# Kernel optimization log

Hardware: AMD Instinct MI355X
Metric: run time of the kernel (lower is better)

## Reference

```python
import jax, jax.numpy as jnp
import numpy as np

B = 16
DRUG_LEN, PROT_LEN = 64, 1200
DIM, CONV = 64, 40


def conv1d(x, w, b):
    # x: [B, C_in, L], w: [C_out, C_in, K] (torch layout), VALID padding
    y = jax.lax.conv_general_dilated(
        x, w, window_strides=(1,), padding='VALID',
        dimension_numbers=('NCH', 'OIH', 'NCH'))
    return y + b[None, :, None]


def setup_inputs() -> dict:
    key = jax.random.key(0)
    ks = jax.random.split(key, 32)
    s = 0.05
    inp = {
        'drug_tokens': jax.random.randint(ks[0], (B, DRUG_LEN), 0, 65, dtype=jnp.int32),
        'protein_tokens': jax.random.randint(ks[1], (B, PROT_LEN), 0, 26, dtype=jnp.int32),
        'drug_emb': (jax.random.normal(ks[2], (65, DIM)) * s).at[0].set(0.0),
        'prot_emb': (jax.random.normal(ks[3], (26, DIM)) * s).at[0].set(0.0),
        'dW1': jax.random.normal(ks[4], (CONV, DIM, 4)) * s,
        'db1': jax.random.normal(ks[5], (CONV,)) * s,
        'dW2': jax.random.normal(ks[6], (CONV * 2, CONV, 6)) * s,
        'db2': jax.random.normal(ks[7], (CONV * 2,)) * s,
        'dW3': jax.random.normal(ks[8], (CONV * 4, CONV * 2, 8)) * s,
        'db3': jax.random.normal(ks[9], (CONV * 4,)) * s,
        'pW1': jax.random.normal(ks[10], (CONV, DIM, 4)) * s,
        'pb1': jax.random.normal(ks[11], (CONV,)) * s,
        'pW2': jax.random.normal(ks[12], (CONV * 2, CONV, 8)) * s,
        'pb2': jax.random.normal(ks[13], (CONV * 2,)) * s,
        'pW3': jax.random.normal(ks[14], (CONV * 4, CONV * 2, 12)) * s,
        'pb3': jax.random.normal(ks[15], (CONV * 4,)) * s,
        'dattW': jax.random.normal(ks[16], (160, 160)) * s,
        'dattb': jax.random.normal(ks[17], (160,)) * s,
        'pattW': jax.random.normal(ks[18], (160, 160)) * s,
        'pattb': jax.random.normal(ks[19], (160,)) * s,
        'attW': jax.random.normal(ks[20], (160, 160)) * s,
        'attb': jax.random.normal(ks[21], (160,)) * s,
        'fc1W': jax.random.normal(ks[22], (1024, 320)) * s,
        'fc1b': jax.random.normal(ks[23], (1024,)) * s,
        'fc2W': jax.random.normal(ks[24], (1024, 1024)) * s,
        'fc2b': jax.random.normal(ks[25], (1024,)) * s,
        'fc3W': jax.random.normal(ks[26], (512, 1024)) * s,
        'fc3b': jax.random.normal(ks[27], (512,)) * s,
        'outW': jax.random.normal(ks[28], (2, 512)) * s,
        'outb': jax.random.normal(ks[29], (2,)) * s,
    }
    return inp


def reference(drug_tokens, protein_tokens, drug_emb, prot_emb,
              dW1, db1, dW2, db2, dW3, db3,
              pW1, pb1, pW2, pb2, pW3, pb3,
              dattW, dattb, pattW, pattb, attW, attb,
              fc1W, fc1b, fc2W, fc2b, fc3W, fc3b, outW, outb):
    relu = jax.nn.relu
    # Embedding lookup, then to [B, C, L]
    de = drug_emb[drug_tokens].transpose(0, 2, 1)    # [B,64,64]
    pe = prot_emb[protein_tokens].transpose(0, 2, 1)  # [B,64,1200]
    # CNN stacks
    dc = relu(conv1d(relu(conv1d(relu(conv1d(de, dW1, db1)), dW2, db2)), dW3, db3))  # [B,160,49]
    pc = relu(conv1d(relu(conv1d(relu(conv1d(pe, pW1, pb1)), pW2, pb2)), pW3, pb3))  # [B,160,1179]
    # Per-token attention projections (Linear over channel dim)
    d_att = jnp.einsum('bcd,oc->bdo', dc, dattW) + dattb   # [B,49,160]
    p_att = jnp.einsum('bcp,oc->bpo', pc, pattW) + pattb   # [B,1179,160]
    # Broadcast outer-sum + ReLU + Linear  -> [B,49,1179,160]
    A = relu(d_att[:, :, None, :] + p_att[:, None, :, :])
    A = jnp.einsum('bdpk,ok->bdpo', A, attW) + attb
    comp_atte = jax.nn.sigmoid(jnp.mean(A, axis=2)).transpose(0, 2, 1)  # [B,160,49]
    prot_atte = jax.nn.sigmoid(jnp.mean(A, axis=1)).transpose(0, 2, 1)  # [B,160,1179]
    dc = dc * 0.5 + dc * comp_atte
    pc = pc * 0.5 + pc * prot_atte
    # Global max pool over length
    dvec = jnp.max(dc, axis=2)  # [B,160]
    pvec = jnp.max(pc, axis=2)  # [B,160]
    pair = jnp.concatenate([dvec, pvec], axis=1)  # [B,320]
    # MLP head (dropout = identity at inference)
    h = jax.nn.leaky_relu(pair @ fc1W.T + fc1b, 0.01)
    h = jax.nn.leaky_relu(h @ fc2W.T + fc2b, 0.01)
    h = jax.nn.leaky_relu(h @ fc3W.T + fc3b, 0.01)
    return h @ outW.T + outb  # [B,2]
```

## Files before the change

kernel.cpp:

```cpp
#include <hip/hip_runtime.h>
#include <hip/hip_bf16.h>

typedef __hip_bfloat16 bf16;
typedef __attribute__((ext_vector_type(8))) short short8;
typedef __attribute__((ext_vector_type(4))) float floatx4;

#define NB 16


__device__ __forceinline__ float b2f(bf16 x) { return __bfloat162float(x); }
__device__ __forceinline__ float u16bf(unsigned short u) {
    return __uint_as_float(((unsigned)u) << 16);
}
__device__ __forceinline__ unsigned short f2bu(float v) {
    union { bf16 h; unsigned short u; } cv;
    cv.h = __float2bfloat16(v);
    return cv.u;
}

__global__ void sniff_kernel(const unsigned short* __restrict__ w, int* __restrict__ flag) {
    __shared__ int cnt;
    if (threadIdx.x == 0) cnt = 0;
    __syncthreads();
    int hits = 0;
    for (int s = 0; s < 4; s++) {
        unsigned short u = w[(threadIdx.x * 4 + s) * 2];
        float v = fabsf(u16bf(u));
        if (v > 1e-6f && v < 2.0f) hits++;
    }
    atomicAdd(&cnt, hits);
    __syncthreads();
    if (threadIdx.x == 0) *flag = (cnt > 512) ? 1 : 0;
}

#define NSEG 14
struct CvtJob {
    const void* src[NSEG];
    float* dst[NSEG];
};
#define NPK 11
struct PackJob {
    const void* src[NPK];
    bf16* dst[NPK];
    short Cout[NPK], CIN[NPK], K[NPK], coP[NPK], CIP[NPK];
};
struct PrepOff { int off[NSEG + NPK + 1]; };

__global__ void prep(CvtJob cj, PackJob pj, PrepOff po, const int* __restrict__ flagp) {
    int g = blockIdx.x * 256 + threadIdx.x;
    if (g >= po.off[NSEG + NPK]) return;
    int s = 0;
#pragma unroll
    for (int t = 1; t < NSEG + NPK; t++)
        if (g >= po.off[t]) s = t;
    int i = g - po.off[s];
    if (s < NSEG) {
        const void* sp = cj.src[s];
        if (sp == nullptr) { cj.dst[s][i] = 0.f; return; }
        cj.dst[s][i] = (*flagp) ? b2f(((const bf16*)sp)[i]) : ((const float*)sp)[i];
    } else {
        int p = s - NSEG;
        int Cout = pj.Cout[p], CIN = pj.CIN[p], K = pj.K[p];
        int coP = pj.coP[p], CIP = pj.CIP[p];
        (void)K;
        int ci = i % CIP;
        int t = i / CIP;
        int co = t % coP;
        int k = t / coP;
        float v = 0.f;
        if (co < Cout && ci < CIN) {
            int si = (co * CIN + ci) * pj.K[p] + k;
            v = (*flagp) ? b2f(((const bf16*)pj.src[p])[si]) : ((const float*)pj.src[p])[si];
        }
        pj.dst[p][i] = __float2bfloat16(v);
    }
}

template <int K, int CIN, int CHUNKS, int NW>
__device__ __forceinline__ void conv_body(unsigned short* xT,
                                          const unsigned short* xb,
                                          const unsigned short* wbase,
                                          const float* __restrict__ bias,
                                          bf16* __restrict__ y,
                                          int b, int Lin, int Lstride, int Lout,
                                          int Cout, int coP, int l0) {
    const int CIP = CHUNKS * 32;
    const int PCI = CIP + 8;
    const int TLX = 64 + K - 1;
    const int LV = (TLX + 7) >> 3;
    for (int i = threadIdx.x; i < CIP * LV; i += NW * 64) {
        int ci = i / LV, lv = (i - ci * LV) << 3;
        if (ci < CIN && lv + 8 <= TLX && l0 + lv + 8 <= Lin) {
            short8 v = *(const short8*)(xb + ci * Lstride + l0 + lv);
#pragma unroll
            for (int j = 0; j < 8; j++) xT[(lv + j) * PCI + ci] = (unsigned short)v[j];
        } else {
            for (int j = 0; j < 8; j++) {
                int l = lv + j;
                if (l >= TLX) break;
                int gl = l0 + l;
                xT[l * PCI + ci] = (ci < CIN && gl < Lin) ? xb[ci * Lstride + gl]
                                                          : (unsigned short)0;
            }
        }
    }
    __syncthreads();
    int lane = threadIdx.x & 63;
    int ct = threadIdx.x >> 6;
    int n = lane & 15, quad = lane >> 4;
    floatx4 acc[4];
#pragma unroll
    for (int i = 0; i < 4; i++) acc[i] = (floatx4){0.f, 0.f, 0.f, 0.f};
#pragma unroll
    for (int k = 0; k < K; k++) {
#pragma unroll
        for (int ch = 0; ch < CHUNKS; ch++) {
            short8 a = *(const short8*)(wbase +
                        ((size_t)(k * coP + ct * 16 + n)) * CIP + ch * 32 + quad * 8);
#pragma unroll
            for (int nt = 0; nt < 4; nt++) {
                short8 bb = *(const short8*)(xT + (nt * 16 + n + k) * PCI + ch * 32 + quad * 8);
                acc[nt] = __builtin_amdgcn_mfma_f32_16x16x32_bf16(a, bb, acc[nt], 0, 0, 0);
            }
        }
    }
    int m0 = quad * 4;
#pragma unroll
    for (int nt = 0; nt < 4; nt++) {
        int l = l0 + nt * 16 + n;
        if (l >= Lout) continue;
#pragma unroll
        for (int r = 0; r < 4; r++) {
            int co = ct * 16 + m0 + r;
            if (co < Cout)
                y[((size_t)b * Cout + co) * Lout + l] =
                    __float2bfloat16(fmaxf(acc[nt][r] + bias[co], 0.f));
        }
    }
}

template <int KD, int KP, int CIN, int CHUNKS, int NW>
__global__ __launch_bounds__(NW * 64) void conv_dual(const bf16* __restrict__ xd,
                                                 const bf16* __restrict__ Wpd,
                                                 const float* __restrict__ bd,
                                                 bf16* __restrict__ yd,
                                                 int LinD, int LsD, int LoutD,
                                                 const bf16* __restrict__ xp,
                                                 const bf16* __restrict__ Wpp,
                                                 const float* __restrict__ bp,
                                                 bf16* __restrict__ yp,
                                                 int LinP, int LsP, int LoutP,
                                                 int Cout, int coP) {
    const int CIP = CHUNKS * 32;
    const int PCI = CIP + 8;
    const int TLXMAX = 64 + KP - 1;
    __shared__ __align__(16) unsigned short xT[TLXMAX * PCI];
    if (blockIdx.x < 16) {
        int b = blockIdx.x;
        conv_body<KD, CIN, CHUNKS, NW>(xT, (const unsigned short*)xd + (size_t)b * CIN * LsD,
                                   (const unsigned short*)Wpd, bd, yd, b, LinD, LsD, LoutD,
                                   Cout, coP, 0);
    } else {
        int bx = blockIdx.x - 16;
        int b = bx / 19, l0 = (bx % 19) << 6;
        conv_body<KP, CIN, CHUNKS, NW>(xT, (const unsigned short*)xp + (size_t)b * CIN * LsP,
                                   (const unsigned short*)Wpp, bp, yp, b, LinP, LsP, LoutP,
                                   Cout, coP, l0);
    }
}

template <int K, int CIN, int CHUNKS, int NW>
__device__ __forceinline__ void conv_proj_phase(unsigned short* xT, unsigned short* xP,
                                                const unsigned short* xb,
                                                const unsigned short* wbase,
                                                const float* __restrict__ bias,
                                                unsigned short* __restrict__ y,
                                                int b, int Lin, int Lout,
                                                int Cout, int coP, int l0) {
    const int CIP = CHUNKS * 32;
    const int PCI = CIP + 8;
    const int TLX = 64 + K - 1;
    const int LV = (TLX + 7) >> 3;
    for (int i = threadIdx.x; i < CIP * LV; i += NW * 64) {
        int ci = i / LV, lv = (i - ci * LV) << 3;
        if (ci < CIN && lv + 8 <= TLX && l0 + lv + 8 <= Lin) {
            short8 v = *(const short8*)(xb + ci * Lin + l0 + lv);
#pragma unroll
            for (int j = 0; j < 8; j++) xT[(lv + j) * PCI + ci] = (unsigned short)v[j];
        } else {
            for (int j = 0; j < 8; j++) {
                int l = lv + j;
                if (l >= TLX) break;
                int gl = l0 + l;
                xT[l * PCI + ci] = (ci < CIN && gl < Lin) ? xb[ci * Lin + gl]
                                                          : (unsigned short)0;
            }
        }
    }
    __syncthreads();
    int lane = threadIdx.x & 63;
    int ct = threadIdx.x >> 6;
    int n = lane & 15, quad = lane >> 4;
    floatx4 acc[4];
#pragma unroll
    for (int i = 0; i < 4; i++) acc[i] = (floatx4){0.f, 0.f, 0.f, 0.f};
#pragma unroll
    for (int k = 0; k < K; k++) {
#pragma unroll
        for (int ch = 0; ch < CHUNKS; ch++) {
            short8 a = *(const short8*)(wbase +
                        ((size_t)(k * coP + ct * 16 + n)) * CIP + ch * 32 + quad * 8);
#pragma unroll
            for (int nt = 0; nt < 4; nt++) {
                short8 bb = *(const short8*)(xT + (nt * 16 + n + k) * PCI + ch * 32 + quad * 8);
                acc[nt] = __builtin_amdgcn_mfma_f32_16x16x32_bf16(a, bb, acc[nt], 0, 0, 0);
            }
        }
    }
    int m0 = quad * 4;
#pragma unroll
    for (int nt = 0; nt < 4; nt++) {
        int ll = nt * 16 + n;
        int l = l0 + ll;
#pragma unroll
        for (int r = 0; r < 4; r++) {
            int co = ct * 16 + m0 + r;
            float val = (l < Lout) ? fmaxf(acc[nt][r] + bias[co], 0.f) : 0.f;
            unsigned short u = f2bu(val);
            xP[ll * 168 + co] = u;
            if (l < Lout) y[((size_t)b * Cout + co) * Lout + l] = u;
        }
    }
}

template <int KD, int KP, int CIN, int CHUNKS, int NW>
__global__ __launch_bounds__(NW * 64) void conv3_proj(
        const bf16* __restrict__ xd, const bf16* __restrict__ Wpd,
        const float* __restrict__ bd, bf16* __restrict__ yd, int LinD, int LoutD,
        const bf16* __restrict__ xp, const bf16* __restrict__ Wpp,
        const float* __restrict__ bp, bf16* __restrict__ yp, int LinP, int LoutP,
        int Cout, int coP,
        const bf16* __restrict__ dWB, const bf16* __restrict__ pWB,
        const float* __restrict__ dbF, const float* __restrict__ pbF,
        float* __restrict__ datt, bf16* __restrict__ pattB) {
    const int CIP = CHUNKS * 32;
    const int PCI = CIP + 8;
    const int TLXMAX = 64 + KP - 1;
    __shared__ __align__(16) unsigned short xT[TLXMAX * PCI];
    __shared__ __align__(16) unsigned short xP[64 * 168];
    bool isD = blockIdx.x < 16;
    int b, l0, L;
    if (isD) {
        b = blockIdx.x; l0 = 0; L = LoutD;
        conv_proj_phase<KD, CIN, CHUNKS, NW>(xT, xP,
            (const unsigned short*)xd + (size_t)b * CIN * LinD,
            (const unsigned short*)Wpd, bd, (unsigned short*)yd, b, LinD, LoutD, Cout, coP, 0);
    } else {
        int bx = blockIdx.x - 16;
        b = bx / 19; l0 = (bx % 19) << 6; L = LoutP;
        conv_proj_phase<KP, CIN, CHUNKS, NW>(xT, xP,
            (const unsigned short*)xp + (size_t)b * CIN * LinP,
            (const unsigned short*)Wpp, bp, (unsigned short*)yp, b, LinP, LoutP, Cout, coP, l0);
    }
    __syncthreads();
    int lane = threadIdx.x & 63;
    int t = threadIdx.x >> 6;
    int n = lane & 15, quad = lane >> 4;
    const unsigned short* W = (const unsigned short*)(isD ? dWB : pWB);
    const float* pbias = isD ? dbF : pbF;
    floatx4 acc[4];
#pragma unroll
    for (int i = 0; i < 4; i++) acc[i] = (floatx4){0.f, 0.f, 0.f, 0.f};
#pragma unroll
    for (int ch = 0; ch < 5; ch++) {
        short8 a = *(const short8*)(W + ((size_t)(t * 16 + n)) * 160 + ch * 32 + quad * 8);
#pragma unroll
        for (int nt = 0; nt < 4; nt++) {
            short8 bb = *(const short8*)(xP + (nt * 16 + n) * 168 + ch * 32 + quad * 8);
            acc[nt] = __builtin_amdgcn_mfma_f32_16x16x32_bf16(a, bb, acc[nt], 0, 0, 0);
        }
    }
    int m0 = quad * 4;
    int o0 = t * 16 + m0;
#pragma unroll
    for (int nt = 0; nt < 4; nt++) {
        int l = l0 + nt * 16 + n;
        if (l >= L) continue;
        if (isD) {
            float4 v;
            v.x = acc[nt][0] + pbias[o0 + 0];
            v.y = acc[nt][1] + pbias[o0 + 1];
            v.z = acc[nt][2] + pbias[o0 + 2];
            v.w = acc[nt][3] + pbias[o0 + 3];
            *(float4*)(datt + ((size_t)b * 49 + l) * 160 + o0) = v;
        } else {
            ushort4 u;
            u.x = f2bu(acc[nt][0] + pbias[o0 + 0]);
            u.y = f2bu(acc[nt][1] + pbias[o0 + 1]);
            u.z = f2bu(acc[nt][2] + pbias[o0 + 2]);
            u.w = f2bu(acc[nt][3] + pbias[o0 + 3]);
            *(ushort4*)((unsigned short*)pattB + ((size_t)b * 1179 + l) * 160 + o0) = u;
        }
    }
}

__global__ __launch_bounds__(256) void conv1_mfma(const int* __restrict__ dtok,
                                                  const int* __restrict__ ptok,
                                                  const bf16* __restrict__ embDB,
                                                  const bf16* __restrict__ embPB,
                                                  const bf16* __restrict__ dW1p,
                                                  const bf16* __restrict__ pW1p,
                                                  const float* __restrict__ db1f,
                                                  const float* __restrict__ pb1f,
                                                  bf16* __restrict__ d1,
                                                  bf16* __restrict__ p1) {
    const int K = 4, CIP = 64, PCI = 72, TLX = 67, coP = 48, Cout = 40;
    __shared__ __align__(16) unsigned short xT[TLX * PCI];
    __shared__ int stok[TLX];
    bool isD = blockIdx.x < 16;
    int b, l0, Lin, Lout, Ostride;
    const int* tok; const unsigned short* embB; const unsigned short* Wp;
    const float* bias; bf16* y;
    if (isD) {
        b = blockIdx.x; l0 = 0; Lin = 64; Lout = 61; Ostride = 62;
        tok = dtok; embB = (const unsigned short*)embDB;
        Wp = (const unsigned short*)dW1p; bias = db1f; y = d1;
    } else {
        int bx = blockIdx.x - 16;
        b = bx / 19; l0 = (bx % 19) << 6; Lin = 1200; Lout = 1197; Ostride = 1198;
        tok = ptok; embB = (const unsigned short*)embPB;
        Wp = (const unsigned short*)pW1p; bias = pb1f; y = p1;
    }
    if (threadIdx.x < TLX) {
        int l = l0 + threadIdx.x;
        stok[threadIdx.x] = (l < Lin) ? tok[b * Lin + l] : -1;
    }
    __syncthreads();
    for (int i = threadIdx.x; i < TLX * 8; i += 256) {
        int l = i >> 3, c8 = (i & 7) << 3;
        int t = stok[l];
        short8 v = (short8){0, 0, 0, 0, 0, 0, 0, 0};
        if (t >= 0) v = *(const short8*)(embB + t * 64 + c8);
        *(short8*)(xT + l * PCI + c8) = v;
    }
    __syncthreads();
    int lane = threadIdx.x & 63;
    int w = threadIdx.x >> 6;
    int n = lane & 15, quad = lane >> 4;
    if (w >= 3) return;
    floatx4 acc[4];
#pragma unroll
    for (int i = 0; i < 4; i++) acc[i] = (floatx4){0.f, 0.f, 0.f, 0.f};
#pragma unroll
    for (int k = 0; k < K; k++) {
#pragma unroll
        for (int ch = 0; ch < 2; ch++) {
            short8 a = *(const short8*)(Wp +
                        ((size_t)(k * coP + w * 16 + n)) * CIP + ch * 32 + quad * 8);
#pragma unroll
            for (int nt = 0; nt < 4; nt++) {
                short8 bb = *(const short8*)(xT + (nt * 16 + n + k) * PCI + ch * 32 + quad * 8);
                acc[nt] = __builtin_amdgcn_mfma_f32_16x16x32_bf16(a, bb, acc[nt], 0, 0, 0);
            }
        }
    }
    int m0 = quad * 4;
#pragma unroll
    for (int nt = 0; nt < 4; nt++) {
        int l = l0 + nt * 16 + n;
        if (l >= Lout) continue;
#pragma unroll
        for (int r = 0; r < 4; r++) {
            int co = w * 16 + m0 + r;
            if (co < Cout)
                y[((size_t)b * Cout + co) * Ostride + l] =
                    __float2bfloat16(fmaxf(acc[nt][r] + bias[co], 0.f));
        }
    }
}

__global__ __launch_bounds__(640) void mean_fused(const float* __restrict__ datt,
                                                  const bf16* __restrict__ patt,
                                                  bf16* __restrict__ MpW,
                                                  float* __restrict__ Mdpart) {
    __shared__ __align__(16) unsigned short sp[37 * 160];
    int tid = threadIdx.x;
    int b = blockIdx.x >> 5;
    int pc = blockIdx.x & 31;
    int p0 = pc * 37;
    int pmax = 1179 - p0;
    if (pmax > 37) pmax = 37;
    {
        const short8* src = (const short8*)((const unsigned short*)patt +
                                            ((size_t)b * 1179 + p0) * 160);
        short8* dst = (short8*)sp;
        int n8 = (pmax * 160) >> 3;
        for (int v = tid; v < n8; v += 640) dst[v] = src[v];
    }
    int h = tid & 3;
    int k = tid >> 2;
    int d0 = h * 13;
    int nd = (h == 3) ? 10 : 13;
    const float* drow = datt + (size_t)b * 49 * 160 + k;
    float dv[13], md[13];
#pragma unroll
    for (int i = 0; i < 13; i++) {
        dv[i] = (i < nd) ? drow[(d0 + i) * 160] : -1e30f;
        md[i] = 0.f;
    }
    __syncthreads();
    unsigned short* mp = (unsigned short*)MpW + ((size_t)b * 1184 + p0) * 160 + k;
#pragma unroll 2
    for (int pi = 0; pi < pmax; pi++) {
        float pv = u16bf(sp[pi * 160 + k]);
        float s0 = 0.f, s1 = 0.f, s2 = 0.f, s3 = 0.f;
#pragma unroll
        for (int g = 0; g < 3; g++) {
            float r0 = fmaxf(dv[g * 4 + 0] + pv, 0.f);
            float r1 = fmaxf(dv[g * 4 + 1] + pv, 0.f);
            float r2 = fmaxf(dv[g * 4 + 2] + pv, 0.f);
            float r3 = fmaxf(dv[g * 4 + 3] + pv, 0.f);
            md[g * 4 + 0] += r0; s0 += r0;
            md[g * 4 + 1] += r1; s1 += r1;
            md[g * 4 + 2] += r2; s2 += r2;
            md[g * 4 + 3] += r3; s3 += r3;
        }
        {
            float r = fmaxf(dv[12] + pv, 0.f);
            md[12] += r; s0 += r;
        }
        float s = (s0 + s1) + (s2 + s3);
        s += __shfl_xor(s, 1, 64);
        s += __shfl_xor(s, 2, 64);
        if (h == 0) mp[(size_t)pi * 160] = f2bu(s * (1.f / 49.f));
    }
    float* op = Mdpart + (((size_t)b * 32 + pc) * 49) * 160 + k;
#pragma unroll
    for (int i = 0; i < 13; i++)
        if (i < nd) op[(d0 + i) * 160] = md[i];
}

__global__ __launch_bounds__(640) void att_sig_mfma(const float* __restrict__ Mdpart,
                                                    const bf16* __restrict__ MpW,
                                                    const bf16* __restrict__ wattB,
                                                    const float* __restrict__ attbF,
                                                    const bf16* __restrict__ dcB,
                                                    const bf16* __restrict__ pcB,
                                                    float* __restrict__ pair) {
    const int PCI = 168;
    __shared__ __align__(16) unsigned short sM[64 * PCI];
    bool isD = blockIdx.x < 16;
    int b, p0, L, off;
    const unsigned short* conv;
    if (isD) {
        b = blockIdx.x; p0 = 0; L = 49; off = 0; conv = (const unsigned short*)dcB;
        const float* mdp = Mdpart + (size_t)b * 32 * 49 * 160;
        for (int i = threadIdx.x; i < 160 * 64; i += 640) {
            int r = i / 160, k = i - r * 160;
            float v = 0.f;
            if (r < 49) {
                const float* src = mdp + r * 160 + k;
                float s0 = 0.f, s1 = 0.f, s2 = 0.f, s3 = 0.f;
#pragma unroll
                for (int pc = 0; pc < 32; pc += 4) {
                    s0 += src[(size_t)(pc + 0) * 7840];
                    s1 += src[(size_t)(pc + 1) * 7840];
                    s2 += src[(size_t)(pc + 2) * 7840];
                    s3 += src[(size_t)(pc + 3) * 7840];
                }
                v = ((s0 + s1) + (s2 + s3)) * (1.f / 1179.f);
            }
            sM[r * PCI + k] = f2bu(v);
        }
    } else {
        int bx = blockIdx.x - 16;
        b = bx / 19; p0 = (bx % 19) << 6; L = 1179; off = 160;
        conv = (const unsigned short*)pcB;
        const unsigned short* mb = (const unsigned short*)MpW + (size_t)b * 1184 * 160;
        for (int i = threadIdx.x; i < 160 * 64; i += 640) {
            int r = i / 160, k = i - r * 160;
            int p = p0 + r;
            sM[r * PCI + k] = (p < 1179) ? mb[(size_t)p * 160 + k] : (unsigned short)0;
        }
    }
    __syncthreads();
    int lane = threadIdx.x & 63;
    int t = threadIdx.x >> 6;
    int n = lane & 15, quad = lane >> 4;
    floatx4 acc[4];
#pragma unroll
    for (int i = 0; i < 4; i++) acc[i] = (floatx4){0.f, 0.f, 0.f, 0.f};
    const unsigned short* W = (const unsigned short*)wattB;
#pragma unroll
    for (int ch = 0; ch < 5; ch++) {
        short8 a = *(const short8*)(W + ((size_t)(t * 16 + n)) * 160 + ch * 32 + quad * 8);
#pragma unroll
        for (int nt = 0; nt < 4; nt++) {
            short8 bb = *(const short8*)(sM + (nt * 16 + n) * PCI + ch * 32 + quad * 8);
            acc[nt] = __builtin_amdgcn_mfma_f32_16x16x32_bf16(a, bb, acc[nt], 0, 0, 0);
        }
    }
    int m0 = quad * 4;
    float vmax[4] = {0.f, 0.f, 0.f, 0.f};
#pragma unroll
    for (int nt = 0; nt < 4; nt++) {
        int p = p0 + nt * 16 + n;
#pragma unroll
        for (int r = 0; r < 4; r++) {
            int o = t * 16 + m0 + r;
            float sig = 1.f / (1.f + __expf(-(acc[nt][r] + attbF[o])));
            float v = 0.f;
            if (p < L) v = u16bf(conv[((size_t)b * 160 + o) * L + p]) * (0.5f + sig);
            vmax[r] = fmaxf(vmax[r], v);
        }
    }
#pragma unroll
    for (int m = 1; m < 16; m <<= 1) {
#pragma unroll
        for (int r = 0; r < 4; r++)
            vmax[r] = fmaxf(vmax[r], __shfl_xor(vmax[r], m, 64));
    }
    if (n == 0) {
#pragma unroll
        for (int r = 0; r < 4; r++)
            atomicMax((unsigned int*)(pair + b * 320 + off + t * 16 + m0 + r),
                      __float_as_uint(vmax[r]));
    }
}

__global__ __launch_bounds__(256) void fc_block(const float* __restrict__ in,
                                                const void* __restrict__ W,
                                                const float* __restrict__ bias,
                                                float* __restrict__ out,
                                                int IN, int OUT,
                                                const int* __restrict__ flagp) {
    int j = blockIdx.x;
    int w = threadIdx.x >> 6, li = threadIdx.x & 63;
    int nv = IN >> 2;
    const float4* i0 = (const float4*)(in + (size_t)(w * 4 + 0) * IN);
    const float4* i1 = (const float4*)(in + (size_t)(w * 4 + 1) * IN);
    const float4* i2 = (const float4*)(in + (size_t)(w * 4 + 2) * IN);
    const float4* i3 = (const float4*)(in + (size_t)(w * 4 + 3) * IN);
    float p0 = 0.f, p1 = 0.f, p2 = 0.f, p3 = 0.f;
    if (*flagp) {
        const ushort4* w4 = (const ushort4*)((const unsigned short*)W + (size_t)j * IN);
        for (int v = li; v < nv; v += 64) {
            ushort4 u = w4[v];
            float wa = u16bf(u.x), wb = u16bf(u.y), wc = u16bf(u.z), wd = u16bf(u.w);
            float4 x;
            x = i0[v]; p0 += x.x * wa + x.y * wb + x.z * wc + x.w * wd;
            x = i1[v]; p1 += x.x * wa + x.y * wb + x.z * wc + x.w * wd;
            x = i2[v]; p2 += x.x * wa + x.y * wb + x.z * wc + x.w * wd;
            x = i3[v]; p3 += x.x * wa + x.y * wb + x.z * wc + x.w * wd;
        }
    } else {
        const float4* w4 = (const float4*)((const float*)W + (size_t)j * IN);
        for (int v = li; v < nv; v += 64) {
            float4 u = w4[v];
            float4 x;
            x = i0[v]; p0 += x.x * u.x + x.y * u.y + x.z * u.z + x.w * u.w;
            x = i1[v]; p1 += x.x * u.x + x.y * u.y + x.z * u.z + x.w * u.w;
            x = i2[v]; p2 += x.x * u.x + x.y * u.y + x.z * u.z + x.w * u.w;
            x = i3[v]; p3 += x.x * u.x + x.y * u.y + x.z * u.z + x.w * u.w;
        }
    }
#pragma unroll
    for (int m = 1; m < 64; m <<= 1) {
        p0 += __shfl_xor(p0, m, 64);
        p1 += __shfl_xor(p1, m, 64);
        p2 += __shfl_xor(p2, m, 64);
        p3 += __shfl_xor(p3, m, 64);
    }
    if (li == 0) {
        float bj = bias[j];
        float o0 = p0 + bj, o1 = p1 + bj, o2 = p2 + bj, o3 = p3 + bj;
        o0 = o0 > 0.f ? o0 : 0.01f * o0;
        o1 = o1 > 0.f ? o1 : 0.01f * o1;
        o2 = o2 > 0.f ? o2 : 0.01f * o2;
        o3 = o3 > 0.f ? o3 : 0.01f * o3;
        out[(size_t)(w * 4 + 0) * OUT + j] = o0;
        out[(size_t)(w * 4 + 1) * OUT + j] = o1;
        out[(size_t)(w * 4 + 2) * OUT + j] = o2;
        out[(size_t)(w * 4 + 3) * OUT + j] = o3;
    }
}

__global__ __launch_bounds__(256) void out_block(const float* __restrict__ h,
                                                 const void* __restrict__ W,
                                                 const float* __restrict__ biasF,
                                                 void* __restrict__ out,
                                                 const int* __restrict__ flagp) {
    int j = blockIdx.x;
    int w = threadIdx.x >> 6, li = threadIdx.x & 63;
    const int IN = 512, nv = 128;
    const float4* i0 = (const float4*)(h + (size_t)(w * 4 + 0) * IN);
    const float4* i1 = (const float4*)(h + (size_t)(w * 4 + 1) * IN);
    const float4* i2 = (const float4*)(h + (size_t)(w * 4 + 2) * IN);
    const float4* i3 = (const float4*)(h + (size_t)(w * 4 + 3) * IN);
    float p0 = 0.f, p1 = 0.f, p2 = 0.f, p3 = 0.f;
    int flag = *flagp;
    if (flag) {
        const ushort4* w4 = (const ushort4*)((const unsigned short*)W + (size_t)j * IN);
        for (int v = li; v < nv; v += 64) {
            ushort4 u = w4[v];
            float wa = u16bf(u.x), wb = u16bf(u.y), wc = u16bf(u.z), wd = u16bf(u.w);
            float4 x;
            x = i0[v]; p0 += x.x * wa + x.y * wb + x.z * wc + x.w * wd;
            x = i1[v]; p1 += x.x * wa + x.y * wb + x.z * wc + x.w * wd;
            x = i2[v]; p2 += x.x * wa + x.y * wb + x.z * wc + x.w * wd;
            x = i3[v]; p3 += x.x * wa + x.y * wb + x.z * wc + x.w * wd;
        }
    } else {
        const float4* w4 = (const float4*)((const float*)W + (size_t)j * IN);
        for (int v = li; v < nv; v += 64) {
            float4 u = w4[v];
            float4 x;
            x = i0[v]; p0 += x.x * u.x + x.y * u.y + x.z * u.z + x.w * u.w;
            x = i1[v]; p1 += x.x * u.x + x.y * u.y + x.z * u.z + x.w * u.w;
            x = i2[v]; p2 += x.x * u.x + x.y * u.y + x.z * u.z + x.w * u.w;
            x = i3[v]; p3 += x.x * u.x + x.y * u.y + x.z * u.z + x.w * u.w;
        }
    }
#pragma unroll
    for (int m = 1; m < 64; m <<= 1) {
        p0 += __shfl_xor(p0, m, 64);
        p1 += __shfl_xor(p1, m, 64);
        p2 += __shfl_xor(p2, m, 64);
        p3 += __shfl_xor(p3, m, 64);
    }
    if (li == 0) {
        float bj = biasF[j];
        float o0 = p0 + bj, o1 = p1 + bj, o2 = p2 + bj, o3 = p3 + bj;
        if (flag) {
            bf16* ob = (bf16*)out;
            ob[(w * 4 + 0) * 2 + j] = __float2bfloat16(o0);
            ob[(w * 4 + 1) * 2 + j] = __float2bfloat16(o1);
            ob[(w * 4 + 2) * 2 + j] = __float2bfloat16(o2);
            ob[(w * 4 + 3) * 2 + j] = __float2bfloat16(o3);
        } else {
            float* of = (float*)out;
            of[(w * 4 + 0) * 2 + j] = o0;
            of[(w * 4 + 1) * 2 + j] = o1;
            of[(w * 4 + 2) * 2 + j] = o2;
            of[(w * 4 + 3) * 2 + j] = o3;
        }
    }
}

extern "C" void kernel_launch(void* const* d_in, const int* in_sizes, int n_in,
                              void* d_out, int out_size, void* d_ws, size_t ws_size,
                              hipStream_t stream) {
    const int* drug_tok = (const int*)d_in[0];
    const int* prot_tok = (const int*)d_in[1];
    const void* drug_emb = d_in[2];
    const void* prot_emb = d_in[3];
    const void* dW1 = d_in[4];  const void* db1 = d_in[5];
    const void* dW2 = d_in[6];  const void* db2 = d_in[7];
    const void* dW3 = d_in[8];  const void* db3 = d_in[9];
    const void* pW1 = d_in[10]; const void* pb1 = d_in[11];
    const void* pW2 = d_in[12]; const void* pb2 = d_in[13];
    const void* pW3 = d_in[14]; const void* pb3 = d_in[15];
    const void* dattW = d_in[16]; const void* dattb = d_in[17];
    const void* pattW = d_in[18]; const void* pattb = d_in[19];
    const void* attW  = d_in[20]; const void* attb  = d_in[21];
    const void* fc1W = d_in[22]; const void* fc1b = d_in[23];
    const void* fc2W = d_in[24]; const void* fc2b = d_in[25];
    const void* fc3W = d_in[26]; const void* fc3b = d_in[27];
    const void* outW = d_in[28]; const void* outb = d_in[29];

    char* base = (char*)d_ws;
    size_t cur = 0;
    auto alloc = [&](size_t bytes) -> char* {
        char* p = base + cur;
        cur = (cur + bytes + 255) & ~(size_t)255;
        return p;
    };
    int*   flag  = (int*)alloc(256);
    bf16* embDB = (bf16*)alloc(65 * 64 * 2);
    bf16* embPB = (bf16*)alloc(26 * 64 * 2);
    bf16* dW1p = (bf16*)alloc((size_t)4 * 48 * 64 * 2);
    bf16* pW1p = (bf16*)alloc((size_t)4 * 48 * 64 * 2);
    bf16* dW2p = (bf16*)alloc((size_t)6 * 128 * 64 * 2);
    bf16* dW3p = (bf16*)alloc((size_t)8 * 192 * 96 * 2);
    bf16* pW2p = (bf16*)alloc((size_t)8 * 128 * 64 * 2);
    bf16* pW3p = (bf16*)alloc((size_t)12 * 192 * 96 * 2);
    float* db1f = (float*)alloc(40 * 4);
    float* db2f = (float*)alloc(80 * 4);
    float* db3f = (float*)alloc(160 * 4);
    float* pb1f = (float*)alloc(40 * 4);
    float* pb2f = (float*)alloc(80 * 4);
    float* pb3f = (float*)alloc(160 * 4);
    float* dattbF = (float*)alloc(160 * 4);
    float* pattbF = (float*)alloc(160 * 4);
    float* attbF  = (float*)alloc(160 * 4);
    float* fc1bF = (float*)alloc(1024 * 4);
    float* fc2bF = (float*)alloc(1024 * 4);
    float* fc3bF = (float*)alloc(512 * 4);
    float* outbF = (float*)alloc(2 * 4);
    bf16* dattWB = (bf16*)alloc(25600 * 2);
    bf16* pattWB = (bf16*)alloc(25600 * 2);
    bf16* wattB  = (bf16*)alloc(25600 * 2);
    bf16* d1  = (bf16*)alloc((size_t)NB * 40 * 62 * 2);
    bf16* d2  = (bf16*)alloc((size_t)NB * 80 * 56 * 2);
    bf16* dcB = (bf16*)alloc((size_t)NB * 160 * 49 * 2);
    bf16* p1  = (bf16*)alloc((size_t)NB * 40 * 1198 * 2);
    bf16* p2  = (bf16*)alloc((size_t)NB * 80 * 1190 * 2);
    bf16* pcB = (bf16*)alloc((size_t)NB * 160 * 1179 * 2);
    float* datt  = (float*)alloc((size_t)NB * 49 * 160 * 4);
    bf16* pattB = (bf16*)alloc((size_t)NB * 1179 * 160 * 2);
    float* Mdpart = (float*)alloc((size_t)NB * 32 * 49 * 160 * 4);
    bf16* MpW  = (bf16*)alloc((size_t)NB * 1184 * 160 * 2);
    float* pair = (float*)alloc(NB * 320 * 4);
    float* h1 = (float*)alloc(NB * 1024 * 4);
    float* h2 = (float*)alloc(NB * 1024 * 4);
    float* h3 = (float*)alloc(NB * 512 * 4);

    sniff_kernel<<<1, 256, 0, stream>>>((const unsigned short*)fc2W, flag);

    CvtJob cj;
    PackJob pj;
    PrepOff po;
    int si = 0, running = 0;
    auto add = [&](const void* s, float* d, int n) {
        cj.src[si] = s; cj.dst[si] = d; po.off[si] = running; running += n; si++;
    };
    add(db1, db1f, 40); add(db2, db2f, 80); add(db3, db3f, 160);
    add(pb1, pb1f, 40); add(pb2, pb2f, 80); add(pb3, pb3f, 160);
    add(dattb, dattbF, 160); add(pattb, pattbF, 160); add(attb, attbF, 160);
    add(fc1b, fc1bF, 1024); add(fc2b, fc2bF, 1024); add(fc3b, fc3bF, 512);
    add(outb, outbF, 2);
    add(nullptr, pair, NB * 320);
    int pi = 0;
    auto seg = [&](const void* s, bf16* d, int Cout, int CIN, int K, int coP, int CIP) {
        pj.src[pi] = s; pj.dst[pi] = d;
        pj.Cout[pi] = Cout; pj.CIN[pi] = CIN; pj.K[pi] = K; pj.coP[pi] = coP; pj.CIP[pi] = CIP;
        po.off[NSEG + pi] = running; running += K * coP * CIP; pi++;
    };
    seg(dW1, dW1p, 40, 64, 4, 48, 64);
    seg(pW1, pW1p, 40, 64, 4, 48, 64);
    seg(dW2, dW2p, 80, 40, 6, 128, 64);
    seg(pW2, pW2p, 80, 40, 8, 128, 64);
    seg(dW3, dW3p, 160, 80, 8, 192, 96);
    seg(pW3, pW3p, 160, 80, 12, 192, 96);
    seg(dattW, dattWB, 160, 160, 1, 160, 160);
    seg(pattW, pattWB, 160, 160, 1, 160, 160);
    seg(attW,  wattB,  160, 160, 1, 160, 160);
    seg(drug_emb, embDB, 65, 64, 1, 65, 64);
    seg(prot_emb, embPB, 26, 64, 1, 26, 64);
    po.off[NSEG + NPK] = running;
    prep<<<(running + 255) / 256, 256, 0, stream>>>(cj, pj, po, flag);

    conv1_mfma<<<16 + 16 * 19, 256, 0, stream>>>(drug_tok, prot_tok, embDB, embPB,
                                                 dW1p, pW1p, db1f, pb1f, d1, p1);
    conv_dual<6, 8, 40, 2, 5><<<320, 320, 0, stream>>>(
        d1, dW2p, db2f, d2, 61, 62, 56,
        p1, pW2p, pb2f, p2, 1197, 1198, 1190, 80, 128);
    conv3_proj<8, 12, 80, 3, 10><<<320, 640, 0, stream>>>(
        d2, dW3p, db3f, dcB, 56, 49,
        p2, pW3p, pb3f, pcB, 1190, 1179, 160, 192,
        dattWB, pattWB, dattbF, pattbF, datt, pattB);

    mean_fused<<<16 * 32, 640, 0, stream>>>(datt, pattB, MpW, Mdpart);

    att_sig_mfma<<<320, 640, 0, stream>>>(Mdpart, MpW, wattB, attbF, dcB, pcB, pair);

    fc_block<<<1024, 256, 0, stream>>>(pair, fc1W, fc1bF, h1, 320, 1024, flag);
    fc_block<<<1024, 256, 0, stream>>>(h1, fc2W, fc2bF, h2, 1024, 1024, flag);
    fc_block<<<512, 256, 0, stream>>>(h2, fc3W, fc3bF, h3, 1024, 512, flag);
    out_block<<<2, 256, 0, stream>>>(h3, outW, outbF, d_out, flag);
}
```

Baseline: 238.9 us.

## Split mean pass into more blocks and add separate drug-mean reduction kernel

Splits the protein-length chunking in mean_fused from 32 chunks of 37 to 48 chunks of 25, which increases the grid to 768 blocks for better occupancy. The reduction of the partial drug means moves out of the 16 drug blocks of att_sig_mfma into a new md_reduce kernel spread over 490 blocks. This removes a serialized tail on those 16 blocks. The protein-side shared-memory load is also vectorized to 16-byte accesses. The cost is an extra kernel launch and a larger partial buffer to write and read.

```diff
diff --git a/kernel.cpp b/kernel.cpp
--- a/kernel.cpp
+++ b/kernel.cpp
@@ -6,6 +6,7 @@
 typedef __attribute__((ext_vector_type(4))) float floatx4;
 
 #define NB 16
+#define NPC 48
 
 
 __device__ __forceinline__ float b2f(bf16 x) { return __bfloat162float(x); }
@@ -60,9 +61,8 @@
         cj.dst[s][i] = (*flagp) ? b2f(((const bf16*)sp)[i]) : ((const float*)sp)[i];
     } else {
         int p = s - NSEG;
-        int Cout = pj.Cout[p], CIN = pj.CIN[p], K = pj.K[p];
+        int Cout = pj.Cout[p], CIN = pj.CIN[p];
         int coP = pj.coP[p], CIP = pj.CIP[p];
-        (void)K;
         int ci = i % CIP;
         int t = i / CIP;
         int co = t % coP;
@@ -383,13 +383,13 @@
                                                   const bf16* __restrict__ patt,
                                                   bf16* __restrict__ MpW,
                                                   float* __restrict__ Mdpart) {
-    __shared__ __align__(16) unsigned short sp[37 * 160];
+    __shared__ __align__(16) unsigned short sp[25 * 160];
     int tid = threadIdx.x;
-    int b = blockIdx.x >> 5;
-    int pc = blockIdx.x & 31;
-    int p0 = pc * 37;
+    int b = blockIdx.x / NPC;
+    int pc = blockIdx.x % NPC;
+    int p0 = pc * 25;
     int pmax = 1179 - p0;
-    if (pmax > 37) pmax = 37;
+    if (pmax > 25) pmax = 25;
     {
         const short8* src = (const short8*)((const unsigned short*)patt +
                                             ((size_t)b * 1179 + p0) * 160);
@@ -434,13 +434,31 @@
         s += __shfl_xor(s, 2, 64);
         if (h == 0) mp[(size_t)pi * 160] = f2bu(s * (1.f / 49.f));
     }
-    float* op = Mdpart + (((size_t)b * 32 + pc) * 49) * 160 + k;
+    float* op = Mdpart + (((size_t)b * NPC + pc) * 49) * 160 + k;
 #pragma unroll
     for (int i = 0; i < 13; i++)
         if (i < nd) op[(d0 + i) * 160] = md[i];
 }
 
-__global__ __launch_bounds__(640) void att_sig_mfma(const float* __restrict__ Mdpart,
+__global__ __launch_bounds__(256) void md_reduce(const float* __restrict__ Mdpart,
+                                                 float* __restrict__ Md) {
+    int i = blockIdx.x * 256 + threadIdx.x;
+    if (i >= NB * 49 * 160) return;
+    int b = i / (49 * 160);
+    int dk = i - b * (49 * 160);
+    const float* src = Mdpart + (size_t)b * NPC * 7840 + dk;
+    float s0 = 0.f, s1 = 0.f, s2 = 0.f, s3 = 0.f;
+#pragma unroll
+    for (int pc = 0; pc < NPC; pc += 4) {
+        s0 += src[(size_t)(pc + 0) * 7840];
+        s1 += src[(size_t)(pc + 1) * 7840];
+        s2 += src[(size_t)(pc + 2) * 7840];
+        s3 += src[(size_t)(pc + 3) * 7840];
+    }
+    Md[i] = (s0 + s1) + (s2 + s3);
+}
+
+__global__ __launch_bounds__(640) void att_sig_mfma(const float* __restrict__ Md,
                                                     const bf16* __restrict__ MpW,
                                                     const bf16* __restrict__ wattB,
                                                     const float* __restrict__ attbF,
@@ -454,22 +472,9 @@
     const unsigned short* conv;
     if (isD) {
         b = blockIdx.x; p0 = 0; L = 49; off = 0; conv = (const unsigned short*)dcB;
-        const float* mdp = Mdpart + (size_t)b * 32 * 49 * 160;
         for (int i = threadIdx.x; i < 160 * 64; i += 640) {
             int r = i / 160, k = i - r * 160;
-            float v = 0.f;
-            if (r < 49) {
-                const float* src = mdp + r * 160 + k;
-                float s0 = 0.f, s1 = 0.f, s2 = 0.f, s3 = 0.f;
-#pragma unroll
-                for (int pc = 0; pc < 32; pc += 4) {
-                    s0 += src[(size_t)(pc + 0) * 7840];
-                    s1 += src[(size_t)(pc + 1) * 7840];
-                    s2 += src[(size_t)(pc + 2) * 7840];
-                    s3 += src[(size_t)(pc + 3) * 7840];
-                }
-                v = ((s0 + s1) + (s2 + s3)) * (1.f / 1179.f);
-            }
+            float v = (r < 49) ? Md[((size_t)b * 49 + r) * 160 + k] * (1.f / 1179.f) : 0.f;
             sM[r * PCI + k] = f2bu(v);
         }
     } else {
@@ -477,10 +482,12 @@
         b = bx / 19; p0 = (bx % 19) << 6; L = 1179; off = 160;
         conv = (const unsigned short*)pcB;
         const unsigned short* mb = (const unsigned short*)MpW + (size_t)b * 1184 * 160;
-        for (int i = threadIdx.x; i < 160 * 64; i += 640) {
-            int r = i / 160, k = i - r * 160;
+        for (int i = threadIdx.x; i < 64 * 20; i += 640) {
+            int r = i / 20, k8 = (i - r * 20) << 3;
             int p = p0 + r;
-            sM[r * PCI + k] = (p < 1179) ? mb[(size_t)p * 160 + k] : (unsigned short)0;
+            short8 v = (short8){0, 0, 0, 0, 0, 0, 0, 0};
+            if (p < 1179) v = *(const short8*)(mb + (size_t)p * 160 + k8);
+            *(short8*)(sM + r * PCI + k8) = v;
         }
     }
     __syncthreads();
@@ -708,7 +715,8 @@
     bf16* pcB = (bf16*)alloc((size_t)NB * 160 * 1179 * 2);
     float* datt  = (float*)alloc((size_t)NB * 49 * 160 * 4);
     bf16* pattB = (bf16*)alloc((size_t)NB * 1179 * 160 * 2);
-    float* Mdpart = (float*)alloc((size_t)NB * 32 * 49 * 160 * 4);
+    float* Md   = (float*)alloc((size_t)NB * 49 * 160 * 4);
+    float* Mdpart = (float*)alloc((size_t)NB * NPC * 49 * 160 * 4);
     bf16* MpW  = (bf16*)alloc((size_t)NB * 1184 * 160 * 2);
     float* pair = (float*)alloc(NB * 320 * 4);
     float* h1 = (float*)alloc(NB * 1024 * 4);
@@ -760,9 +768,10 @@
         p2, pW3p, pb3f, pcB, 1190, 1179, 160, 192,
         dattWB, pattWB, dattbF, pattbF, datt, pattB);
 
-    mean_fused<<<16 * 32, 640, 0, stream>>>(datt, pattB, MpW, Mdpart);
-
-    att_sig_mfma<<<320, 640, 0, stream>>>(Mdpart, MpW, wattB, attbF, dcB, pcB, pair);
+    mean_fused<<<16 * NPC, 640, 0, stream>>>(datt, pattB, MpW, Mdpart);
+    md_reduce<<<490, 256, 0, stream>>>(Mdpart, Md);
+
+    att_sig_mfma<<<320, 640, 0, stream>>>(Md, MpW, wattB, attbF, dcB, pcB, pair);
 
     fc_block<<<1024, 256, 0, stream>>>(pair, fc1W, fc1bF, h1, 320, 1024, flag);
     fc_block<<<1024, 256, 0, stream>>>(h1, fc2W, fc2bF, h2, 1024, 1024, flag);
```

Measured after the change: 223.9 us (median of 2 runs). 1.07x faster.
